# Optimization experiments

Hardware: AMD Instinct MI355X
Metric: run time of the kernel (lower is better)

The kernel has to match this reference:

```python
import jax, jax.numpy as jnp
import numpy as np

B, N, A = 8, 16384, 7
NUM_GROUP = 1024   # npoint / G
GROUP_SIZE = 32    # knn k / M


def setup_inputs() -> dict:
    key = jax.random.key(0)
    xyz = jax.random.uniform(key, (B, N, A), dtype=jnp.float32)
    return {"xyz": xyz}


def _farthest_point_sample(xyz, npoint):
    # xyz: [B, N, A]; distances computed on first 3 dims only.
    b, n, a = xyz.shape
    coords = xyz[:, :, :3]
    batch = jnp.arange(b)
    # Deterministic start index (original uses randint; any start is a valid FPS seed).
    init = (jnp.full((b, n), 1e10, dtype=xyz.dtype), jnp.zeros((b,), dtype=jnp.int32))

    def step(carry, _):
        distance, farthest = carry
        centroid = xyz[batch, farthest]                      # [B, A]
        d = jnp.sum((coords - centroid[:, None, :3]) ** 2, -1)  # [B, N]
        distance = jnp.minimum(distance, d)                  # masked update == min
        new_farthest = jnp.argmax(distance, axis=-1).astype(jnp.int32)
        return (distance, new_farthest), (farthest, centroid)

    _, (idxs, cents) = jax.lax.scan(step, init, None, length=npoint)
    centroids = jnp.swapaxes(idxs, 0, 1)        # [B, npoint]
    centroids_attrs = jnp.swapaxes(cents, 0, 1)  # [B, npoint, A]
    return centroids, centroids_attrs


def _knn(center, xyz, k):
    # Euclidean cdist over ALL A attributes (as in the original torch.cdist call).
    # Squared distance preserves topk ordering.
    c2 = jnp.sum(center ** 2, -1)[:, :, None]    # [B, G, 1]
    x2 = jnp.sum(xyz ** 2, -1)[:, None, :]       # [B, 1, N]
    d2 = c2 + x2 - 2.0 * jnp.einsum('bga,bna->bgn', center, xyz)  # [B, G, N]
    _, idx = jax.lax.top_k(-d2, k)               # smallest-k, ascending distance
    return idx


def reference(xyz):
    center_idx, centroids_attrs = _farthest_point_sample(xyz, NUM_GROUP)
    centroids_coors = centroids_attrs[:, :, :3]
    idx = _knn(centroids_attrs, xyz, GROUP_SIZE)             # [B, G, M]
    b = xyz.shape[0]
    neighborhood = xyz[jnp.arange(b)[:, None, None], idx]    # [B, G, M, A]
    neighborhood = jnp.concatenate(
        [neighborhood[..., :3] - centroids_coors[:, :, None, :],
         neighborhood[..., 3:]], axis=-1)
    return neighborhood, center_idx, centroids_attrs, centroids_coors
```

## Files before the change

### kernel.cpp

```cpp
#include <hip/hip_runtime.h>

#define N_PTS  16384
#define B_SZ   8
#define NGROUP 1024
#define KNN_K  32
#define ATTR   7

#define OFF_NB     0
#define OFF_IDX    (B_SZ * NGROUP * KNN_K * ATTR)
#define OFF_CATTR  (OFF_IDX + B_SZ * NGROUP)
#define OFF_CCOORD (OFF_CATTR + B_SZ * NGROUP * ATTR)

typedef float v2f __attribute__((ext_vector_type(2)));
typedef float f2u __attribute__((ext_vector_type(2), aligned(4)));

__global__ void prep_kernel(const float* __restrict__ xyz, float* __restrict__ x2,
                            float* __restrict__ xt) {
#pragma clang fp contract(off)
    int i = blockIdx.x * blockDim.x + threadIdx.x;
    if (i >= B_SZ * N_PTS) return;
    const int b = i >> 14;
    const int p = i & (N_PTS - 1);
    const float* q = xyz + (size_t)i * ATTR;
    f2u a01 = *(const f2u*)q;
    f2u a23 = *(const f2u*)(q + 2);
    f2u a45 = *(const f2u*)(q + 4);
    float a6 = q[6];
    float s = a01.x * a01.x;
    s = s + a01.y * a01.y;
    s = s + a23.x * a23.x;
    s = s + a23.y * a23.y;
    s = s + a45.x * a45.x;
    s = s + a45.y * a45.y;
    s = s + a6 * a6;
    x2[i] = s;
    float* T = xt + (size_t)b * ATTR * N_PTS + p;
    T[0 * N_PTS] = a01.x;
    T[1 * N_PTS] = a01.y;
    T[2 * N_PTS] = a23.x;
    T[3 * N_PTS] = a23.y;
    T[4 * N_PTS] = a45.x;
    T[5 * N_PTS] = a45.y;
    T[6 * N_PTS] = a6;
}

__global__ __launch_bounds__(1024) void fps_kernel(const float* __restrict__ xyz,
                                                   float* __restrict__ out) {
#pragma clang fp contract(off)
    const int b = blockIdx.x;
    const int t = threadIdx.x;
    const int lane = t & 63;
    const float* X = xyz + (size_t)b * N_PTS * ATTR;

    v2f px[8], py[8], pz[8], pd[8];
#pragma unroll
    for (int j = 0; j < 8; ++j) {
        const int p0 = t + (j << 11);
        const float* q0 = X + (size_t)p0 * ATTR;
        const float* q1 = q0 + (size_t)1024 * ATTR;
        f2u u0 = *(const f2u*)q0; float z0 = q0[2];
        f2u u1 = *(const f2u*)q1; float z1 = q1[2];
        px[j] = (v2f){u0.x, u1.x};
        py[j] = (v2f){u0.y, u1.y};
        pz[j] = (v2f){z0, z1};
        pd[j] = (v2f){1e10f, 1e10f};
    }

    __shared__ unsigned long long slot[3];
    __shared__ int sel[NGROUP];
    if (t == 0) { slot[0] = 0ull; sel[0] = 0; }
    float cx = X[0], cy = X[1], cz = X[2];
    __syncthreads();

    for (int s = 0; s < NGROUP - 1; ++s) {
        const v2f cx2 = {cx, cx}, cy2 = {cy, cy}, cz2 = {cz, cz};
        float best = -1.0f;
        int   bidx = 0;
#pragma unroll
        for (int j = 0; j < 8; ++j) {
            v2f dx = px[j] - cx2;
            v2f dy = py[j] - cy2;
            v2f dz = pz[j] - cz2;
            v2f a  = dx * dx;
            a = a + dy * dy;
            a = a + dz * dz;
            v2f nd;
            nd.x = fminf(pd[j].x, a.x);
            nd.y = fminf(pd[j].y, a.y);
            pd[j] = nd;
            if (nd.x > best) { best = nd.x; bidx = t + ((2 * j) << 10); }
            if (nd.y > best) { best = nd.y; bidx = t + ((2 * j + 1) << 10); }
        }
        unsigned long long key =
            ((unsigned long long)__float_as_uint(best) << 32) |
            (unsigned)(N_PTS - bidx);
#pragma unroll
        for (int off = 1; off < 64; off <<= 1) {
            unsigned long long ok = __shfl_xor(key, off);
            if (ok > key) key = ok;
        }
        if (lane == 0) atomicMax(&slot[s % 3], key);
        if (t == 0) slot[(s + 1) % 3] = 0ull;
        __syncthreads();
        key = slot[s % 3];
        const int lo = (int)(unsigned)key;
        bidx = N_PTS - __builtin_amdgcn_readfirstlane(lo);
        if (t == 0) sel[s + 1] = bidx;
        const float* q = X + (size_t)bidx * ATTR;
        cx = q[0]; cy = q[1]; cz = q[2];
    }
    __syncthreads();

    {
        const int g = t;
        const int idx = sel[g];
        const float* q = X + (size_t)idx * ATTR;
        float a0 = q[0], a1 = q[1], a2 = q[2], a3 = q[3], a4 = q[4], a5 = q[5], a6 = q[6];
        out[OFF_IDX + b * NGROUP + g] = (float)idx;
        float* ca = out + OFF_CATTR + (size_t)(b * NGROUP + g) * ATTR;
        ca[0] = a0; ca[1] = a1; ca[2] = a2; ca[3] = a3; ca[4] = a4; ca[5] = a5; ca[6] = a6;
        float* cc = out + OFF_CCOORD + (size_t)(b * NGROUP + g) * 3;
        cc[0] = a0; cc[1] = a1; cc[2] = a2;
    }
}

__device__ __forceinline__ void topk_insert(float d2, int p, int lane,
                                            float& ld, int& li, float& kd, int& ki) {
    const bool cand = (d2 < kd) || (d2 == kd && p < ki);
    unsigned long long mask = __ballot(cand);
    while (mask) {
        const int l = __ffsll(mask) - 1;
        mask &= mask - 1;
        const float dc = __shfl(d2, l);
        const int   pc = __shfl(p, l);
        if ((dc < kd) || (dc == kd && pc < ki)) {
            const bool before = (ld < dc) || (ld == dc && li < pc);
            const int pos = (int)__popcll(__ballot(before));
            const float sd = __shfl_up(ld, 1);
            const int   si = __shfl_up(li, 1);
            if (lane == pos)      { ld = dc; li = pc; }
            else if (lane > pos)  { ld = sd; li = si; }
            if (lane >= KNN_K)    { ld = __builtin_inff(); li = 0x7fffffff; }
            kd = __shfl(ld, KNN_K - 1);
            ki = __shfl(li, KNN_K - 1);
        }
    }
}

__global__ __launch_bounds__(256) void knn_kernel(const float* __restrict__ xyz,
                                                  const float* __restrict__ x2,
                                                  const float* __restrict__ xt,
                                                  float* __restrict__ out) {
#pragma clang fp contract(off)
    const int lane = threadIdx.x & 63;
    const int gg = blockIdx.x * 4 + (threadIdx.x >> 6);
    const int b  = gg >> 10;
    const float* X = xyz + (size_t)b * N_PTS * ATTR;

    const float* C = out + OFF_CATTR + (size_t)gg * ATTR;
    const float c0 = C[0], c1 = C[1], c2a = C[2], c3 = C[3], c4 = C[4], c5 = C[5], c6 = C[6];
    float csq = c0 * c0;
    csq = csq + c1 * c1;
    csq = csq + c2a * c2a;
    csq = csq + c3 * c3;
    csq = csq + c4 * c4;
    csq = csq + c5 * c5;
    csq = csq + c6 * c6;

    float ld = __builtin_inff();
    int   li = 0x7fffffff;
    float kd = __builtin_inff();
    int   ki = 0x7fffffff;

    if (xt != nullptr) {
        const float* T0 = xt + (size_t)b * ATTR * N_PTS;
        const float* T1 = T0 + N_PTS;
        const float* T2 = T1 + N_PTS;
        const float* T3 = T2 + N_PTS;
        const float* T4 = T3 + N_PTS;
        const float* T5 = T4 + N_PTS;
        const float* T6 = T5 + N_PTS;
        const float* XB = x2 + (size_t)b * N_PTS;
        for (int p0 = 0; p0 < N_PTS; p0 += 64) {
            const int p = p0 + lane;
            const float q0 = T0[p], q1 = T1[p], q2 = T2[p], q3 = T3[p];
            const float q4 = T4[p], q5 = T5[p], q6 = T6[p];
            float dot = c0 * q0;
            dot = dot + c1 * q1;
            dot = dot + c2a * q2;
            dot = dot + c3 * q3;
            dot = dot + c4 * q4;
            dot = dot + c5 * q5;
            dot = dot + c6 * q6;
            const float xx = XB[p];
            const float d2 = (csq + xx) - 2.0f * dot;
            topk_insert(d2, p, lane, ld, li, kd, ki);
        }
    } else {
        for (int p0 = 0; p0 < N_PTS; p0 += 64) {
            const int p = p0 + lane;
            const float* q = X + (size_t)p * ATTR;
            float dot = c0 * q[0];
            dot = dot + c1 * q[1];
            dot = dot + c2a * q[2];
            dot = dot + c3 * q[3];
            dot = dot + c4 * q[4];
            dot = dot + c5 * q[5];
            dot = dot + c6 * q[6];
            float xx = q[0] * q[0];
            xx = xx + q[1] * q[1];
            xx = xx + q[2] * q[2];
            xx = xx + q[3] * q[3];
            xx = xx + q[4] * q[4];
            xx = xx + q[5] * q[5];
            xx = xx + q[6] * q[6];
            const float d2 = (csq + xx) - 2.0f * dot;
            topk_insert(d2, p, lane, ld, li, kd, ki);
        }
    }

    if (lane < KNN_K) {
        const float* q = X + (size_t)li * ATTR;
        float* o = out + OFF_NB + ((size_t)gg * KNN_K + lane) * ATTR;
        o[0] = q[0] - c0;
        o[1] = q[1] - c1;
        o[2] = q[2] - c2a;
        o[3] = q[3];
        o[4] = q[4];
        o[5] = q[5];
        o[6] = q[6];
    }
}

extern "C" void kernel_launch(void* const* d_in, const int* in_sizes, int n_in,
                              void* d_out, int out_size, void* d_ws, size_t ws_size,
                              hipStream_t stream) {
    const float* xyz = (const float*)d_in[0];
    float* out = (float*)d_out;

    const size_t need = (size_t)(B_SZ * N_PTS) * (1 + ATTR) * sizeof(float);
    const bool use_ws = ws_size >= need;
    float* x2 = use_ws ? (float*)d_ws : nullptr;
    float* xt = use_ws ? ((float*)d_ws + B_SZ * N_PTS) : nullptr;

    if (use_ws) {
        prep_kernel<<<(B_SZ * N_PTS + 255) / 256, 256, 0, stream>>>(xyz, x2, xt);
    }
    fps_kernel<<<B_SZ, 1024, 0, stream>>>(xyz, out);
    knn_kernel<<<(B_SZ * NGROUP) / 4, 256, 0, stream>>>(xyz, x2, xt, out);
}
```

Before: 2.197 ms.

## Shrink FPS block to 512 threads and use DPP wave reductions

The FPS kernel now runs 512 threads per batch, each holding 32 points in registers. The 64-bit shuffle-xor argmax is replaced by a DPP float max followed by a DPP unsigned min on the index. The shared-memory atomicMax slot becomes a double-buffered per-wave array that every thread scans after the single barrier. The aim is to shorten the per-iteration reduction and barrier cost on the serial 1023-step loop, at the cost of more register pressure and more arithmetic per thread.

```diff
diff --git a/kernel.cpp b/kernel.cpp
--- a/kernel.cpp
+++ b/kernel.cpp
@@ -13,6 +13,38 @@
 
 typedef float v2f __attribute__((ext_vector_type(2)));
 typedef float f2u __attribute__((ext_vector_type(2), aligned(4)));
+
+template <int CTRL>
+__device__ __forceinline__ float fmax_dpp_step(float x) {
+    int d = __builtin_amdgcn_update_dpp(__float_as_int(x), __float_as_int(x),
+                                        CTRL, 0xf, 0xf, false);
+    return fmaxf(x, __int_as_float(d));
+}
+template <int CTRL>
+__device__ __forceinline__ unsigned umin_dpp_step(unsigned x) {
+    unsigned d = (unsigned)__builtin_amdgcn_update_dpp((int)x, (int)x,
+                                                       CTRL, 0xf, 0xf, false);
+    return x < d ? x : d;
+}
+
+__device__ __forceinline__ float wave_max_f32(float x) {
+    x = fmax_dpp_step<0x111>(x);
+    x = fmax_dpp_step<0x112>(x);
+    x = fmax_dpp_step<0x114>(x);
+    x = fmax_dpp_step<0x118>(x);
+    x = fmax_dpp_step<0x142>(x);
+    x = fmax_dpp_step<0x143>(x);
+    return __int_as_float(__builtin_amdgcn_readlane(__float_as_int(x), 63));
+}
+__device__ __forceinline__ unsigned wave_min_u32(unsigned x) {
+    x = umin_dpp_step<0x111>(x);
+    x = umin_dpp_step<0x112>(x);
+    x = umin_dpp_step<0x114>(x);
+    x = umin_dpp_step<0x118>(x);
+    x = umin_dpp_step<0x142>(x);
+    x = umin_dpp_step<0x143>(x);
+    return (unsigned)__builtin_amdgcn_readlane((int)x, 63);
+}
 
 __global__ void prep_kernel(const float* __restrict__ xyz, float* __restrict__ x2,
                             float* __restrict__ xt) {
@@ -44,20 +76,21 @@
     T[6 * N_PTS] = a6;
 }
 
-__global__ __launch_bounds__(1024) void fps_kernel(const float* __restrict__ xyz,
-                                                   float* __restrict__ out) {
+__global__ __launch_bounds__(512, 2) void fps_kernel(const float* __restrict__ xyz,
+                                                     float* __restrict__ out) {
 #pragma clang fp contract(off)
     const int b = blockIdx.x;
     const int t = threadIdx.x;
     const int lane = t & 63;
+    const int w = t >> 6;
     const float* X = xyz + (size_t)b * N_PTS * ATTR;
 
-    v2f px[8], py[8], pz[8], pd[8];
+    v2f px[16], py[16], pz[16], pd[16];
 #pragma unroll
-    for (int j = 0; j < 8; ++j) {
-        const int p0 = t + (j << 11);
+    for (int j = 0; j < 16; ++j) {
+        const int p0 = t + (j << 10);
         const float* q0 = X + (size_t)p0 * ATTR;
-        const float* q1 = q0 + (size_t)1024 * ATTR;
+        const float* q1 = q0 + (size_t)512 * ATTR;
         f2u u0 = *(const f2u*)q0; float z0 = q0[2];
         f2u u1 = *(const f2u*)q1; float z1 = q1[2];
         px[j] = (v2f){u0.x, u1.x};
@@ -66,18 +99,19 @@
         pd[j] = (v2f){1e10f, 1e10f};
     }
 
-    __shared__ unsigned long long slot[3];
+    __shared__ unsigned long long sbuf[2][8];
     __shared__ int sel[NGROUP];
-    if (t == 0) { slot[0] = 0ull; sel[0] = 0; }
+    if (t == 0) sel[0] = 0;
     float cx = X[0], cy = X[1], cz = X[2];
     __syncthreads();
 
     for (int s = 0; s < NGROUP - 1; ++s) {
+        const int par = s & 1;
         const v2f cx2 = {cx, cx}, cy2 = {cy, cy}, cz2 = {cz, cz};
         float best = -1.0f;
         int   bidx = 0;
 #pragma unroll
-        for (int j = 0; j < 8; ++j) {
+        for (int j = 0; j < 16; ++j) {
             v2f dx = px[j] - cx2;
             v2f dy = py[j] - cy2;
             v2f dz = pz[j] - cz2;
@@ -88,31 +122,32 @@
             nd.x = fminf(pd[j].x, a.x);
             nd.y = fminf(pd[j].y, a.y);
             pd[j] = nd;
-            if (nd.x > best) { best = nd.x; bidx = t + ((2 * j) << 10); }
-            if (nd.y > best) { best = nd.y; bidx = t + ((2 * j + 1) << 10); }
-        }
-        unsigned long long key =
-            ((unsigned long long)__float_as_uint(best) << 32) |
-            (unsigned)(N_PTS - bidx);
+            if (nd.x > best) { best = nd.x; bidx = t + ((2 * j) << 9); }
+            if (nd.y > best) { best = nd.y; bidx = t + ((2 * j + 1) << 9); }
+        }
+        const float wm = wave_max_f32(best);
+        const unsigned cand = (best == wm) ? (unsigned)bidx : 0xFFFFFFFFu;
+        const unsigned widx = wave_min_u32(cand);
+        if (lane == 0) {
+            sbuf[par][w] = ((unsigned long long)__float_as_uint(wm) << 32) |
+                           (unsigned)(N_PTS - widx);
+        }
+        __syncthreads();
+        unsigned long long bk = sbuf[par][0];
 #pragma unroll
-        for (int off = 1; off < 64; off <<= 1) {
-            unsigned long long ok = __shfl_xor(key, off);
-            if (ok > key) key = ok;
-        }
-        if (lane == 0) atomicMax(&slot[s % 3], key);
-        if (t == 0) slot[(s + 1) % 3] = 0ull;
-        __syncthreads();
-        key = slot[s % 3];
-        const int lo = (int)(unsigned)key;
-        bidx = N_PTS - __builtin_amdgcn_readfirstlane(lo);
-        if (t == 0) sel[s + 1] = bidx;
-        const float* q = X + (size_t)bidx * ATTR;
+        for (int i = 1; i < 8; ++i) {
+            const unsigned long long k = sbuf[par][i];
+            if (k > bk) bk = k;
+        }
+        const int win = N_PTS - (int)(unsigned)bk;
+        const int sbidx = __builtin_amdgcn_readfirstlane(win);
+        if (t == 0) sel[s + 1] = sbidx;
+        const float* q = X + (size_t)sbidx * ATTR;
         cx = q[0]; cy = q[1]; cz = q[2];
     }
     __syncthreads();
 
-    {
-        const int g = t;
+    for (int g = t; g < NGROUP; g += 512) {
         const int idx = sel[g];
         const float* q = X + (size_t)idx * ATTR;
         float a0 = q[0], a1 = q[1], a2 = q[2], a3 = q[3], a4 = q[4], a5 = q[5], a6 = q[6];
@@ -246,6 +281,6 @@
     if (use_ws) {
         prep_kernel<<<(B_SZ * N_PTS + 255) / 256, 256, 0, stream>>>(xyz, x2, xt);
     }
-    fps_kernel<<<B_SZ, 1024, 0, stream>>>(xyz, out);
+    fps_kernel<<<B_SZ, 512, 0, stream>>>(xyz, out);
     knn_kernel<<<(B_SZ * NGROUP) / 4, 256, 0, stream>>>(xyz, x2, xt, out);
 }
```

New measurement: 1.998 ms. 1.1x faster.
